# Optimization experiments

Measured on AMD Instinct MI355X. Metric: run time of the kernel, lower is better.

The kernel has to match this reference:

```python
import jax, jax.numpy as jnp
import numpy as np

B, S, HID = 1, 1024, 4096
NH, NKV, HD = 32, 8, 128
GROUPS = NH // NKV
THETA = 10000.0
SPAR = 0.5          # sparse_aggression (layer_idx > 0)
MIN_IDX = 4         # min_sparse_index: always-kept sink tokens
NEG = jnp.float32(-1e30)


def setup_inputs() -> dict:
    key = jax.random.key(0)
    k0, k1, k2, k3, k4 = jax.random.split(key, 5)
    sc = 0.02
    return {
        "hidden_states": jax.random.normal(k0, (B, S, HID), jnp.float32),
        "position_ids": jnp.arange(S, dtype=jnp.int32)[None, :],
        "Wq": jax.random.normal(k1, (NH * HD, HID), jnp.float32) * sc,
        "Wk": jax.random.normal(k2, (NKV * HD, HID), jnp.float32) * sc,
        "Wv": jax.random.normal(k3, (NKV * HD, HID), jnp.float32) * sc,
        "Wo": jax.random.normal(k4, (HID, NH * HD), jnp.float32) * sc,
    }


def _rotate_half(x):
    h = x.shape[-1] // 2
    return jnp.concatenate([-x[..., h:], x[..., :h]], axis=-1)


def _rope_cos_sin(position_ids):
    inv_freq = 1.0 / (THETA ** (jnp.arange(0, HD, 2, dtype=jnp.float32) / HD))
    freqs = position_ids.astype(jnp.float32)[..., None] * inv_freq  # [B,S,HD/2]
    emb = jnp.concatenate([freqs, freqs], axis=-1)                  # [B,S,HD]
    return jnp.cos(emb)[:, None], jnp.sin(emb)[:, None]             # [B,1,S,HD]


def reference(hidden_states, position_ids, Wq, Wk, Wv, Wo):
    b, s, _ = hidden_states.shape
    # QKV projections (nn.Linear: x @ W.T)
    q = (hidden_states @ Wq.T).reshape(b, s, NH, HD).transpose(0, 2, 1, 3)
    k = (hidden_states @ Wk.T).reshape(b, s, NKV, HD).transpose(0, 2, 1, 3)
    v = (hidden_states @ Wv.T).reshape(b, s, NKV, HD).transpose(0, 2, 1, 3)
    # RoPE
    cos, sin = _rope_cos_sin(position_ids)
    q = q * cos + _rotate_half(q) * sin
    k = k * cos + _rotate_half(k) * sin
    # repeat_kv (GQA expansion)
    k = jnp.repeat(k, GROUPS, axis=1)
    v = jnp.repeat(v, GROUPS, axis=1)
    # causal additive mask [1,1,S,S]
    causal = jnp.where(jnp.triu(jnp.ones((s, s), bool), 1), NEG, jnp.float32(0))[None, None]
    scale = 1.0 / np.sqrt(HD)
    scores = jnp.einsum('bhqd,bhkd->bhqk', q, k) * scale
    # oracle importance: softmax of (softmaxed) masked attention (no_grad in original)
    oracle = jax.nn.softmax((scores + causal).astype(jnp.float32), axis=-1)
    importance = jax.nn.softmax(oracle, axis=-1)
    importance = jax.lax.stop_gradient(importance)
    # descending sort -> rank of each key for each query
    sorted_idx = jnp.argsort(-importance, axis=-1)          # [B,H,S,S]
    ranks = jnp.argsort(sorted_idx, axis=-1)                # inverse perm
    # per-query token budget: keep ceil-ish top-k proportional to row length
    k_per_row = jnp.maximum((SPAR * (jnp.arange(s) + 1)).astype(jnp.int32), 1)
    key_idx = jnp.arange(s)
    kept = (ranks < k_per_row[None, None, :, None]) | (key_idx[None, None, None, :] < MIN_IDX)
    sparse_mask = jnp.where(kept, jnp.float32(0), NEG)
    # sparse attention
    attn = scores + sparse_mask + causal
    probs = jax.nn.softmax(attn.astype(jnp.float32), axis=-1).astype(v.dtype)
    out = jnp.einsum('bhqk,bhkd->bhqd', probs, v)           # [B,H,S,HD]
    out = out.transpose(0, 2, 1, 3).reshape(b, s, NH * HD)
    return out @ Wo.T
```

## Files before the change

kernel.cpp:

```cpp
#include <hip/hip_runtime.h>
#include <hip/hip_bf16.h>

#define S_LEN 1024
#define HID   4096
#define NH    32
#define NKV   8
#define HD    128
#define MIN_IDX 4
#define AO_COLS 4096
#define HEAD_STRIDE 131072

typedef __attribute__((ext_vector_type(8))) short short8;
typedef __attribute__((ext_vector_type(4))) float f32x4;

__device__ __forceinline__ unsigned short f2bf(float f) {
  union { float f; unsigned u; } v; v.f = f;
  unsigned r = v.u + 0x7FFFu + ((v.u >> 16) & 1u);
  return (unsigned short)(r >> 16);
}
__device__ __forceinline__ float bf2f(unsigned short h) {
  union { unsigned u; float f; } v; v.u = ((unsigned)h) << 16;
  return v.f;
}
__device__ __forceinline__ unsigned pk2(float a, float b) {
  union { __hip_bfloat162 h; unsigned u; } c;
  c.h = __float22bfloat162_rn(make_float2(a, b));
  return c.u;
}
__device__ __forceinline__ short8 pack8(float4 a, float4 b) {
  union { short8 s; unsigned u[4]; } r;
  r.u[0] = pk2(a.x, a.y); r.u[1] = pk2(a.z, a.w);
  r.u[2] = pk2(b.x, b.y); r.u[3] = pk2(b.z, b.w);
  return r.s;
}
__device__ __forceinline__ unsigned ordf(float f) {
  union { float f; int i; } v; v.f = f;
  return (unsigned)(v.i ^ ((v.i >> 31) | 0x80000000));
}
__device__ __forceinline__ float iordf(unsigned u) {
  union { int i; float f; } v;
  v.i = (u & 0x80000000u) ? (int)(u ^ 0x80000000u) : (int)~u;
  return v.f;
}
__device__ __forceinline__ float wave_sum_f(float v) {
  #pragma unroll
  for (int m = 32; m >= 1; m >>= 1) v += __shfl_xor(v, m);
  return v;
}
__device__ __forceinline__ unsigned wave_max_u(unsigned v) {
  #pragma unroll
  for (int m = 32; m >= 1; m >>= 1) { unsigned o = __shfl_xor(v, m); v = o > v ? o : v; }
  return v;
}
__device__ __forceinline__ void wave_lds_fence() {
  __builtin_amdgcn_s_waitcnt(0xC07F);
  __builtin_amdgcn_wave_barrier();
}
__device__ __forceinline__ void gload_lds16(const unsigned short* g, unsigned short* l) {
  auto gp = (const __attribute__((address_space(1))) unsigned*)g;
  auto lp = (__attribute__((address_space(3))) unsigned*)(unsigned)(unsigned long long)l;
  __builtin_amdgcn_global_load_lds(gp, lp, 16, 0, 0);
}

__global__ __launch_bounds__(256) void cvt_k(
    const float* __restrict__ src, unsigned short* __restrict__ dst)
{
  const size_t i = ((size_t)blockIdx.x * 256 + threadIdx.x) * 8;
  float4 a = *(const float4*)(src + i);
  float4 b = *(const float4*)(src + i + 4);
  *(short8*)(dst + i) = pack8(a, b);
}

__global__ __launch_bounds__(256) void gemm_qkv_k(
    const unsigned short* __restrict__ Xb, const unsigned short* __restrict__ Wb,
    unsigned short* __restrict__ Qraw, unsigned short* __restrict__ Kraw,
    unsigned short* __restrict__ Vt)
{
  __shared__ unsigned short As[128 * 32];
  __shared__ unsigned short Bs[128 * 32];
  const int nt = blockIdx.x;
  const int n0 = nt * 128;
  const int m0 = blockIdx.y * 128;
  const int t = threadIdx.x, w = t >> 6, lane = t & 63;
  const int wm = w >> 1, wn = w & 1;
  const int mcol = lane & 15, quad = lane >> 4;
  const int lrow = lane >> 2, lcol = (lane & 3) * 8;

  const unsigned short* Ag = Xb + (size_t)m0 * HID;
  const unsigned short* Bg = Wb + (size_t)n0 * HID;

  f32x4 acc[4][4];
  #pragma unroll
  for (int i = 0; i < 4; i++)
    #pragma unroll
    for (int j = 0; j < 4; j++) acc[i][j] = (f32x4){0.f, 0.f, 0.f, 0.f};

  for (int k0 = 0; k0 < HID; k0 += 32) {
    #pragma unroll
    for (int c2 = 0; c2 < 2; c2++) {
      const int c = w * 2 + c2;
      gload_lds16(Ag + (size_t)(c*16 + lrow) * HID + k0 + lcol, &As[c * 512]);
      gload_lds16(Bg + (size_t)(c*16 + lrow) * HID + k0 + lcol, &Bs[c * 512]);
    }
    __syncthreads();
    short8 af[4], bf[4];
    #pragma unroll
    for (int i = 0; i < 4; i++) af[i] = *(const short8*)&As[(wm*64 + i*16 + mcol)*32 + quad*8];
    #pragma unroll
    for (int j = 0; j < 4; j++) bf[j] = *(const short8*)&Bs[(wn*64 + j*16 + mcol)*32 + quad*8];
    #pragma unroll
    for (int i = 0; i < 4; i++)
      #pragma unroll
      for (int j = 0; j < 4; j++)
        acc[i][j] = __builtin_amdgcn_mfma_f32_16x16x32_bf16(af[i], bf[j], acc[i][j], 0, 0, 0);
    __syncthreads();
  }

  if (nt < 40) {
    unsigned short* dst = (nt < 32) ? (Qraw + (size_t)nt * HEAD_STRIDE)
                                    : (Kraw + (size_t)(nt - 32) * HEAD_STRIDE);
    #pragma unroll
    for (int i = 0; i < 4; i++) {
      const int rb = m0 + wm*64 + i*16 + quad*4;
      #pragma unroll
      for (int j = 0; j < 4; j++) {
        const int d = wn*64 + j*16 + mcol;
        #pragma unroll
        for (int r = 0; r < 4; r++)
          dst[(size_t)(rb + r) * HD + d] = f2bf(acc[i][j][r]);
      }
    }
  } else {
    unsigned short* dst = Vt + (size_t)(nt - 40) * HEAD_STRIDE;
    #pragma unroll
    for (int i = 0; i < 4; i++) {
      const int rb = m0 + wm*64 + i*16 + quad*4;
      #pragma unroll
      for (int j = 0; j < 4; j++) {
        const int d = wn*64 + j*16 + mcol;
        ushort4 v4;
        v4.x = f2bf(acc[i][j][0]); v4.y = f2bf(acc[i][j][1]);
        v4.z = f2bf(acc[i][j][2]); v4.w = f2bf(acc[i][j][3]);
        *(ushort4*)(dst + (size_t)d * S_LEN + rb) = v4;
      }
    }
  }
}

__global__ __launch_bounds__(256) void rope_qk_k(
    const int* __restrict__ pos_ids,
    unsigned short* __restrict__ Qraw, unsigned short* __restrict__ Kraw)
{
  const int w = threadIdx.x >> 6, lane = threadIdx.x & 63;
  const int gw = blockIdx.x * 4 + w;
  const int hidx = gw >> 10;
  const int s = gw & 1023;
  const float pos = (float)pos_ids[s];
  const float invf = powf(10000.0f, -(float)lane * (1.0f / 64.0f));
  float sn, cs;
  sincosf(pos * invf, &sn, &cs);
  unsigned short* base = (hidx < NH)
      ? (Qraw + (size_t)hidx * HEAD_STRIDE + (size_t)s * HD)
      : (Kraw + (size_t)(hidx - NH) * HEAD_STRIDE + (size_t)s * HD);
  const float x0 = bf2f(base[lane]), x1 = bf2f(base[lane + 64]);
  base[lane]      = f2bf(x0 * cs - x1 * sn);
  base[lane + 64] = f2bf(x1 * cs + x0 * sn);
}

#define PSTR 1040
template<int KT>
__device__ __forceinline__ void attn_body(
    const unsigned short* __restrict__ Qb, const unsigned short* __restrict__ Kh,
    const unsigned short* __restrict__ Vh, unsigned short* __restrict__ AO,
    unsigned short (*Pl)[PSTR], unsigned (*hist)[256], float* rowinv,
    int q0, int h, int w, int lane, int mcol, int quad)
{
  constexpr int NC = 2 * KT;
  const float scale = 0.08838834764831845f;
  float (*scb)[16][130] = (float (*)[16][130])&Pl[0][0];

  short8 aq[4];
  {
    const unsigned short* qrow = Qb + ((size_t)h * S_LEN + q0 + mcol) * HD + quad * 8;
    #pragma unroll
    for (int kk = 0; kk < 4; kk++) aq[kk] = *(const short8*)(qrow + kk * 32);
  }

  unsigned su[4][NC];

  #pragma unroll
  for (int kt = 0; kt < KT; kt++) {
    short8 bfr[2][4];
    #pragma unroll
    for (int g2 = 0; g2 < 2; g2++) {
      const int key = kt * 128 + (w * 2 + g2) * 16 + mcol;
      const unsigned short* krow = Kh + (size_t)key * HD + quad * 8;
      #pragma unroll
      for (int kk = 0; kk < 4; kk++) bfr[g2][kk] = *(const short8*)(krow + kk * 32);
    }
    f32x4 d4[2];
    d4[0] = (f32x4){0.f,0.f,0.f,0.f}; d4[1] = (f32x4){0.f,0.f,0.f,0.f};
    #pragma unroll
    for (int g2 = 0; g2 < 2; g2++)
      #pragma unroll
      for (int kk = 0; kk < 4; kk++)
        d4[g2] = __builtin_amdgcn_mfma_f32_16x16x32_bf16(aq[kk], bfr[g2][kk], d4[g2], 0, 0, 0);
    #pragma unroll
    for (int g2 = 0; g2 < 2; g2++) {
      const int colc = (w * 2 + g2) * 16 + mcol;
      #pragma unroll
      for (int r = 0; r < 4; r++) scb[kt & 1][quad*4 + r][colc] = d4[g2][r] * scale;
    }
    __syncthreads();
    #pragma unroll
    for (int i = 0; i < 4; i++)
      #pragma unroll
      for (int sub = 0; sub < 2; sub++)
        su[i][kt*2 + sub] = ordf(scb[kt & 1][w*4 + i][sub*64 + lane]);
  }
  __syncthreads();

  const unsigned long long lmlt = (1ull << lane) - 1ull;
  int Lr[4], krem[4], tot[4];
  unsigned prefix[4];
  #pragma unroll
  for (int i = 0; i < 4; i++) {
    Lr[i] = q0 + w*4 + i + 1;
    int ks = Lr[i] >> 1; if (ks < 1) ks = 1;
    krem[i] = ks; tot[i] = Lr[i]; prefix[i] = 0u;
  }

  unsigned msk = 0u;
  #pragma unroll
  for (int pass = 0; pass < 2; pass++) {
    const int shift = 24 - pass * 8;
    #pragma unroll
    for (int p = 0; p < 2; p++) {
      { uint4 z = {0u, 0u, 0u, 0u}; *(uint4*)&hist[w][lane * 4] = z; }
      wave_lds_fence();
      #pragma unroll
      for (int c = 0; c < NC; c++) {
        const int j = c * 64 + lane;
        #pragma unroll
        for (int rr = 0; rr < 2; rr++) {
          const int i = p * 2 + rr;
          if (j < Lr[i] && (su[i][c] & msk) == prefix[i])
            atomicAdd(&hist[w][(su[i][c] >> shift) & 255], 1u << (16 * rr));
        }
      }
      wave_lds_fence();
      const uint4 cv = *(const uint4*)&hist[w][252 - lane * 4];
      unsigned c4[4] = { cv.w, cv.z, cv.y, cv.x };
      const unsigned lsum = c4[0] + c4[1] + c4[2] + c4[3];
      unsigned x = lsum;
      #pragma unroll
      for (int d2 = 1; d2 < 64; d2 <<= 1) { unsigned y = __shfl_up(x, d2); if (lane >= d2) x += y; }
      const unsigned runp = x - lsum;
      #pragma unroll
      for (int rr = 0; rr < 2; rr++) {
        const int i = p * 2 + rr;
        const int sh16 = 16 * rr;
        int run = (int)((runp >> sh16) & 0xFFFFu);
        int fbin = -1, fbefore = 0, fcnt = 0;
        #pragma unroll
        for (int j2 = 0; j2 < 4; j2++) {
          const int cnum = (int)((c4[j2] >> sh16) & 0xFFFFu);
          if (fbin < 0 && run < krem[i] && run + cnum >= krem[i]) {
            fbin = 255 - lane*4 - j2; fbefore = run; fcnt = cnum;
          }
          run += cnum;
        }
        const unsigned long long bal = __ballot(fbin >= 0);
        int bin = 0, before = 0, cnt = krem[i];
        if (bal != 0ull) {
          const int srcl = __ffsll((unsigned long long)bal) - 1;
          bin = __shfl(fbin, srcl);
          before = __shfl(fbefore, srcl);
          cnt = __shfl(fcnt, srcl);
          if (bin < 0) bin = 0;
        }
        krem[i] -= before; if (krem[i] < 1) krem[i] = 1;
        tot[i] = cnt;
        prefix[i] |= ((unsigned)bin) << shift;
      }
    }
    msk |= 0xFFu << (24 - pass * 8);
  }

  #pragma unroll
  for (int i = 0; i < 4; i++) {
    const int r = w * 4 + i;
    const int L = Lr[i];
    unsigned btau = prefix[i];
    unsigned bmsk = 0xFFFF0000u;
    int kr = krem[i];
    int tt = tot[i];
    #pragma unroll 1
    for (int b = 15; b >= 0; --b) {
      if (tt <= kr) break;
      const unsigned bit = 1u << b;
      const unsigned am = bmsk | bit;
      const unsigned test = btau | bit;
      int cnt = 0;
      #pragma unroll
      for (int c = 0; c < NC; c++) {
        const int j = c * 64 + lane;
        cnt += (int)__popcll(__ballot(j < L && (su[i][c] & am) == test));
      }
      if (cnt >= kr) { btau = test; tt = cnt; }
      else           { kr -= cnt; tt -= cnt; }
      bmsk = am;
    }

    unsigned um = 0;
    #pragma unroll
    for (int c = 0; c < NC; c++) {
      const int j = c * 64 + lane;
      if (j < L && su[i][c] > um) um = su[i][c];
    }
    const float mx = iordf(wave_max_u(um));

    float ssum = 0.f;
    int tiebase = 0;
    #pragma unroll
    for (int c = 0; c < NC; c++) {
      const int j = c * 64 + lane;
      const unsigned u = su[i][c];
      const unsigned umv = u & bmsk;
      const bool eq = (j < L) && (umv == btau);
      const unsigned long long bal = __ballot(eq);
      const int trank = tiebase + (int)__popcll(bal & lmlt);
      tiebase += (int)__popcll(bal);
      const bool kept = (j < L) &&
          ((umv > btau) || (eq && trank < kr) || (j < MIN_IDX));
      const float e = kept ? __expf(iordf(u) - mx) : 0.f;
      Pl[r][c*64 + lane] = f2bf(e);
      ssum += e;
    }
    ssum = wave_sum_f(ssum);
    if (lane == 0) rowinv[r] = 1.f / fmaxf(ssum, 1e-30f);
  }
  __syncthreads();

  f32x4 opv[2];
  opv[0] = (f32x4){0.f,0.f,0.f,0.f}; opv[1] = (f32x4){0.f,0.f,0.f,0.f};
  #pragma unroll
  for (int kt = 0; kt < KT; kt++) {
    #pragma unroll
    for (int kb = 0; kb < 4; kb++) {
      short8 af = *(const short8*)&Pl[mcol][kt*128 + kb*32 + quad*8];
      #pragma unroll
      for (int n2 = 0; n2 < 2; n2++) {
        const int d = (w*2 + n2) * 16 + mcol;
        short8 bfr = *(const short8*)(Vh + (size_t)d * S_LEN + kt*128 + kb*32 + quad*8);
        opv[n2] = __builtin_amdgcn_mfma_f32_16x16x32_bf16(af, bfr, opv[n2], 0, 0, 0);
      }
    }
  }
  #pragma unroll
  for (int n2 = 0; n2 < 2; n2++) {
    const int col = h * HD + (w*2 + n2) * 16 + mcol;
    #pragma unroll
    for (int r2 = 0; r2 < 4; r2++) {
      const int row = q0 + quad*4 + r2;
      AO[(size_t)row * AO_COLS + col] = f2bf(opv[n2][r2] * rowinv[quad*4 + r2]);
    }
  }
}

__global__ __launch_bounds__(256, 4) void attn_k(
    const unsigned short* __restrict__ Qb, const unsigned short* __restrict__ Kb,
    const unsigned short* __restrict__ Vt, unsigned short* __restrict__ AO)
{
  __shared__ unsigned short Pl[16][PSTR];
  __shared__ unsigned hist[4][256];
  __shared__ float rowinv[16];
  const int rb = (int)gridDim.x - 1 - (int)blockIdx.x;
  const int h = blockIdx.y;
  const int kvh = h >> 2;
  const int q0 = rb * 16;
  const int kt_max = (rb >> 3) + 1;
  const int t = threadIdx.x, w = t >> 6, lane = t & 63;
  const int mcol = lane & 15, quad = lane >> 4;
  const unsigned short* Kh = Kb + (size_t)kvh * HEAD_STRIDE;
  const unsigned short* Vh = Vt + (size_t)kvh * HEAD_STRIDE;

  switch (kt_max) {
    case 1: attn_body<1>(Qb, Kh, Vh, AO, Pl, hist, rowinv, q0, h, w, lane, mcol, quad); break;
    case 2: attn_body<2>(Qb, Kh, Vh, AO, Pl, hist, rowinv, q0, h, w, lane, mcol, quad); break;
    case 3: attn_body<3>(Qb, Kh, Vh, AO, Pl, hist, rowinv, q0, h, w, lane, mcol, quad); break;
    case 4: attn_body<4>(Qb, Kh, Vh, AO, Pl, hist, rowinv, q0, h, w, lane, mcol, quad); break;
    case 5: attn_body<5>(Qb, Kh, Vh, AO, Pl, hist, rowinv, q0, h, w, lane, mcol, quad); break;
    case 6: attn_body<6>(Qb, Kh, Vh, AO, Pl, hist, rowinv, q0, h, w, lane, mcol, quad); break;
    case 7: attn_body<7>(Qb, Kh, Vh, AO, Pl, hist, rowinv, q0, h, w, lane, mcol, quad); break;
    default: attn_body<8>(Qb, Kh, Vh, AO, Pl, hist, rowinv, q0, h, w, lane, mcol, quad); break;
  }
}

__global__ __launch_bounds__(256) void gemm_out_k(
    const unsigned short* __restrict__ A, const unsigned short* __restrict__ Wob,
    float* __restrict__ Out)
{
  __shared__ unsigned short As[128 * 32];
  __shared__ unsigned short Bs[128 * 32];
  const int n0 = blockIdx.x * 128;
  const int m0 = blockIdx.y * 128;
  const int t = threadIdx.x, w = t >> 6, lane = t & 63;
  const int wm = w >> 1, wn = w & 1;
  const int mcol = lane & 15, quad = lane >> 4;
  const int lrow = lane >> 2, lcol = (lane & 3) * 8;

  const unsigned short* Ag = A   + (size_t)m0 * AO_COLS;
  const unsigned short* Bg = Wob + (size_t)n0 * AO_COLS;

  f32x4 acc[4][4];
  #pragma unroll
  for (int i = 0; i < 4; i++)
    #pragma unroll
    for (int j = 0; j < 4; j++) acc[i][j] = (f32x4){0.f, 0.f, 0.f, 0.f};

  for (int k0 = 0; k0 < AO_COLS; k0 += 32) {
    #pragma unroll
    for (int c2 = 0; c2 < 2; c2++) {
      const int c = w * 2 + c2;
      gload_lds16(Ag + (size_t)(c*16 + lrow) * AO_COLS + k0 + lcol, &As[c * 512]);
      gload_lds16(Bg + (size_t)(c*16 + lrow) * AO_COLS + k0 + lcol, &Bs[c * 512]);
    }
    __syncthreads();
    short8 af[4], bf[4];
    #pragma unroll
    for (int i = 0; i < 4; i++) af[i] = *(const short8*)&As[(wm*64 + i*16 + mcol)*32 + quad*8];
    #pragma unroll
    for (int j = 0; j < 4; j++) bf[j] = *(const short8*)&Bs[(wn*64 + j*16 + mcol)*32 + quad*8];
    #pragma unroll
    for (int i = 0; i < 4; i++)
      #pragma unroll
      for (int j = 0; j < 4; j++)
        acc[i][j] = __builtin_amdgcn_mfma_f32_16x16x32_bf16(af[i], bf[j], acc[i][j], 0, 0, 0);
    __syncthreads();
  }
  #pragma unroll
  for (int i = 0; i < 4; i++) {
    const int rb = m0 + wm*64 + i*16 + quad*4;
    #pragma unroll
    for (int j = 0; j < 4; j++) {
      const int col = n0 + wn*64 + j*16 + mcol;
      #pragma unroll
      for (int r = 0; r < 4; r++)
        Out[(size_t)(rb + r) * HID + col] = acc[i][j][r];
    }
  }
}

extern "C" void kernel_launch(void* const* d_in, const int* in_sizes, int n_in,
                              void* d_out, int out_size, void* d_ws, size_t ws_size,
                              hipStream_t stream) {
  (void)in_sizes; (void)n_in; (void)out_size; (void)ws_size;
  const float* X   = (const float*)d_in[0];
  const int*   pos = (const int*)d_in[1];
  const float* Wq  = (const float*)d_in[2];
  const float* Wk  = (const float*)d_in[3];
  const float* Wv  = (const float*)d_in[4];
  const float* Wo  = (const float*)d_in[5];
  float* out = (float*)d_out;

  char* ws = (char*)d_ws;
  unsigned short* Qraw  = (unsigned short*)ws;
  unsigned short* Kraw  = (unsigned short*)(ws + 8388608);
  unsigned short* Vt    = (unsigned short*)(ws + 10485760);
  unsigned short* AO    = (unsigned short*)(ws + 12582912);
  unsigned short* Xb    = (unsigned short*)(ws + 20971520);
  unsigned short* Wqkvb = (unsigned short*)(ws + 29360128);
  unsigned short* Wob   = Wqkvb;

  cvt_k<<<dim3(2048), dim3(256), 0, stream>>>(X,  Xb);
  cvt_k<<<dim3(8192), dim3(256), 0, stream>>>(Wq, Wqkvb);
  cvt_k<<<dim3(2048), dim3(256), 0, stream>>>(Wk, Wqkvb + 16777216);
  cvt_k<<<dim3(2048), dim3(256), 0, stream>>>(Wv, Wqkvb + 20971520);

  gemm_qkv_k<<<dim3(48, 8),  dim3(256), 0, stream>>>(Xb, Wqkvb, Qraw, Kraw, Vt);
  rope_qk_k <<<dim3(10240),  dim3(256), 0, stream>>>(pos, Qraw, Kraw);

  cvt_k<<<dim3(8192), dim3(256), 0, stream>>>(Wo, Wob);

  attn_k    <<<dim3(64, 32), dim3(256), 0, stream>>>(Qraw, Kraw, Vt, AO);
  gemm_out_k<<<dim3(32, 8),  dim3(256), 0, stream>>>(AO, Wob, out);
}
```

Before: 537.2 us.

## Triple-buffer GEMM loads, fuse input conversions, and tighten radix top-k select

Both GEMM kernels move to a three-stage LDS ring with async global-to-LDS loads issued two tiles ahead. This replaces the two syncthreads per k-step with one vmcnt wait and one barrier, so memory latency overlaps with MFMA work. The four fp32-to-bf16 conversion launches become one kernel that picks its source by block index, saving launch overhead. The top-k radix select in attention now uses three 6-bit passes with a lane-replicated histogram to cut atomic contention, and skips rows whose threshold is already resolved. The cost is more LDS per GEMM block, which may lower occupancy, plus more complex select logic.

New measurement: 456.4 us. 15.0% less time.

```diff
diff --git a/kernel.cpp b/kernel.cpp
--- a/kernel.cpp
+++ b/kernel.cpp
@@ -71,13 +71,30 @@
   *(short8*)(dst + i) = pack8(a, b);
 }
 
+__global__ __launch_bounds__(256) void cvt4_k(
+    const float* __restrict__ s0, const float* __restrict__ s1,
+    const float* __restrict__ s2, const float* __restrict__ s3,
+    unsigned short* __restrict__ d0, unsigned short* __restrict__ d1)
+{
+  const int b = blockIdx.x;
+  const float* src; unsigned short* dst; int rb;
+  if (b < 2048)       { src = s0; dst = d0;            rb = b; }
+  else if (b < 10240) { src = s1; dst = d1;            rb = b - 2048; }
+  else if (b < 12288) { src = s2; dst = d1 + 16777216; rb = b - 10240; }
+  else                { src = s3; dst = d1 + 20971520; rb = b - 12288; }
+  const size_t i = ((size_t)rb * 256 + threadIdx.x) * 8;
+  float4 a = *(const float4*)(src + i);
+  float4 c = *(const float4*)(src + i + 4);
+  *(short8*)(dst + i) = pack8(a, c);
+}
+
 __global__ __launch_bounds__(256) void gemm_qkv_k(
     const unsigned short* __restrict__ Xb, const unsigned short* __restrict__ Wb,
     unsigned short* __restrict__ Qraw, unsigned short* __restrict__ Kraw,
     unsigned short* __restrict__ Vt)
 {
-  __shared__ unsigned short As[128 * 32];
-  __shared__ unsigned short Bs[128 * 32];
+  __shared__ unsigned short As[3][128 * 32];
+  __shared__ unsigned short Bs[3][128 * 32];
   const int nt = blockIdx.x;
   const int n0 = nt * 128;
   const int m0 = blockIdx.y * 128;
@@ -95,25 +112,39 @@
     #pragma unroll
     for (int j = 0; j < 4; j++) acc[i][j] = (f32x4){0.f, 0.f, 0.f, 0.f};
 
-  for (int k0 = 0; k0 < HID; k0 += 32) {
-    #pragma unroll
-    for (int c2 = 0; c2 < 2; c2++) {
-      const int c = w * 2 + c2;
-      gload_lds16(Ag + (size_t)(c*16 + lrow) * HID + k0 + lcol, &As[c * 512]);
-      gload_lds16(Bg + (size_t)(c*16 + lrow) * HID + k0 + lcol, &Bs[c * 512]);
-    }
-    __syncthreads();
+  constexpr int NT = HID / 32;
+  #define STAGE_QKV(buf, k0)                                                  \
+    { const int c0 = w * 2, c1 = w * 2 + 1;                                   \
+      gload_lds16(Ag + (size_t)(c0*16 + lrow) * HID + (k0) + lcol, &As[buf][c0 * 512]); \
+      gload_lds16(Bg + (size_t)(c0*16 + lrow) * HID + (k0) + lcol, &Bs[buf][c0 * 512]); \
+      gload_lds16(Ag + (size_t)(c1*16 + lrow) * HID + (k0) + lcol, &As[buf][c1 * 512]); \
+      gload_lds16(Bg + (size_t)(c1*16 + lrow) * HID + (k0) + lcol, &Bs[buf][c1 * 512]); }
+
+  STAGE_QKV(0, 0)
+  STAGE_QKV(1, 32)
+  asm volatile("s_waitcnt vmcnt(4)" ::: "memory");
+  __builtin_amdgcn_s_barrier();
+  __builtin_amdgcn_sched_barrier(0);
+
+  int cur = 0, stg = 2;
+  for (int kt = 0; kt < NT; ++kt) {
+    if (kt + 2 < NT) STAGE_QKV(stg, (kt + 2) * 32)
     short8 af[4], bf[4];
     #pragma unroll
-    for (int i = 0; i < 4; i++) af[i] = *(const short8*)&As[(wm*64 + i*16 + mcol)*32 + quad*8];
-    #pragma unroll
-    for (int j = 0; j < 4; j++) bf[j] = *(const short8*)&Bs[(wn*64 + j*16 + mcol)*32 + quad*8];
+    for (int i = 0; i < 4; i++) af[i] = *(const short8*)&As[cur][(wm*64 + i*16 + mcol)*32 + quad*8];
+    #pragma unroll
+    for (int j = 0; j < 4; j++) bf[j] = *(const short8*)&Bs[cur][(wn*64 + j*16 + mcol)*32 + quad*8];
     #pragma unroll
     for (int i = 0; i < 4; i++)
       #pragma unroll
       for (int j = 0; j < 4; j++)
         acc[i][j] = __builtin_amdgcn_mfma_f32_16x16x32_bf16(af[i], bf[j], acc[i][j], 0, 0, 0);
-    __syncthreads();
+    if (kt + 2 < NT) { asm volatile("s_waitcnt vmcnt(4)" ::: "memory"); }
+    else             { asm volatile("s_waitcnt vmcnt(0)" ::: "memory"); }
+    __builtin_amdgcn_s_barrier();
+    __builtin_amdgcn_sched_barrier(0);
+    cur = (cur == 2) ? 0 : cur + 1;
+    stg = (stg == 2) ? 0 : stg + 1;
   }
 
   if (nt < 40) {
@@ -221,21 +252,23 @@
   __syncthreads();
 
   const unsigned long long lmlt = (1ull << lane) - 1ull;
+  const int rep = lane & 3;
   int Lr[4], krem[4], tot[4];
-  unsigned prefix[4];
+  unsigned prefix[4], pmsk[4];
   #pragma unroll
   for (int i = 0; i < 4; i++) {
     Lr[i] = q0 + w*4 + i + 1;
     int ks = Lr[i] >> 1; if (ks < 1) ks = 1;
-    krem[i] = ks; tot[i] = Lr[i]; prefix[i] = 0u;
-  }
-
-  unsigned msk = 0u;
-  #pragma unroll
-  for (int pass = 0; pass < 2; pass++) {
-    const int shift = 24 - pass * 8;
+    krem[i] = ks; tot[i] = Lr[i]; prefix[i] = 0u; pmsk[i] = 0u;
+  }
+
+  #pragma unroll
+  for (int pass = 0; pass < 3; pass++) {
+    const int shift = 26 - pass * 6;
     #pragma unroll
     for (int p = 0; p < 2; p++) {
+      const int i0 = p*2, i1 = p*2 + 1;
+      if (tot[i0] <= krem[i0] && tot[i1] <= krem[i1]) continue;
       { uint4 z = {0u, 0u, 0u, 0u}; *(uint4*)&hist[w][lane * 4] = z; }
       wave_lds_fence();
       #pragma unroll
@@ -244,47 +277,39 @@
         #pragma unroll
         for (int rr = 0; rr < 2; rr++) {
           const int i = p * 2 + rr;
-          if (j < Lr[i] && (su[i][c] & msk) == prefix[i])
-            atomicAdd(&hist[w][(su[i][c] >> shift) & 255], 1u << (16 * rr));
+          if (tot[i] > krem[i] && j < Lr[i] && (su[i][c] & pmsk[i]) == prefix[i])
+            atomicAdd(&hist[w][((su[i][c] >> shift) & 63) * 4 + rep], 1u << (16 * rr));
         }
       }
       wave_lds_fence();
-      const uint4 cv = *(const uint4*)&hist[w][252 - lane * 4];
-      unsigned c4[4] = { cv.w, cv.z, cv.y, cv.x };
-      const unsigned lsum = c4[0] + c4[1] + c4[2] + c4[3];
-      unsigned x = lsum;
+      const uint4 cv = *(const uint4*)&hist[w][(63 - lane) * 4];
+      const unsigned cnt2 = cv.x + cv.y + cv.z + cv.w;
+      unsigned x = cnt2;
       #pragma unroll
       for (int d2 = 1; d2 < 64; d2 <<= 1) { unsigned y = __shfl_up(x, d2); if (lane >= d2) x += y; }
-      const unsigned runp = x - lsum;
+      const unsigned runp = x - cnt2;
       #pragma unroll
       for (int rr = 0; rr < 2; rr++) {
         const int i = p * 2 + rr;
+        if (tot[i] <= krem[i]) continue;
         const int sh16 = 16 * rr;
-        int run = (int)((runp >> sh16) & 0xFFFFu);
-        int fbin = -1, fbefore = 0, fcnt = 0;
-        #pragma unroll
-        for (int j2 = 0; j2 < 4; j2++) {
-          const int cnum = (int)((c4[j2] >> sh16) & 0xFFFFu);
-          if (fbin < 0 && run < krem[i] && run + cnum >= krem[i]) {
-            fbin = 255 - lane*4 - j2; fbefore = run; fcnt = cnum;
-          }
-          run += cnum;
-        }
-        const unsigned long long bal = __ballot(fbin >= 0);
-        int bin = 0, before = 0, cnt = krem[i];
-        if (bal != 0ull) {
-          const int srcl = __ffsll((unsigned long long)bal) - 1;
-          bin = __shfl(fbin, srcl);
-          before = __shfl(fbefore, srcl);
-          cnt = __shfl(fcnt, srcl);
-          if (bin < 0) bin = 0;
-        }
-        krem[i] -= before; if (krem[i] < 1) krem[i] = 1;
-        tot[i] = cnt;
+        const int run = (int)((runp >> sh16) & 0xFFFFu);
+        const int cn  = (int)((cnt2 >> sh16) & 0xFFFFu);
+        const bool hit = (run < krem[i]) && (run + cn >= krem[i]);
+        unsigned packv = hit ? (((unsigned)(63 - lane) << 22) |
+                                ((unsigned)run << 11) | (unsigned)cn) : 0u;
+        const unsigned long long bal = __ballot(hit);
+        const int srcl = __ffsll(bal) - 1;
+        const unsigned res = __shfl(packv, srcl);
+        const int bin = res >> 22;
+        const int before = (res >> 11) & 0x7FF;
+        const int cn2 = res & 0x7FF;
+        krem[i] -= before;
+        tot[i] = cn2;
         prefix[i] |= ((unsigned)bin) << shift;
+        pmsk[i] |= 63u << shift;
       }
     }
-    msk |= 0xFFu << (24 - pass * 8);
   }
 
   #pragma unroll
@@ -292,11 +317,12 @@
     const int r = w * 4 + i;
     const int L = Lr[i];
     unsigned btau = prefix[i];
-    unsigned bmsk = 0xFFFF0000u;
+    unsigned bmsk = pmsk[i];
     int kr = krem[i];
     int tt = tot[i];
+    const int bs = (bmsk == 0u) ? 31 : (__builtin_ctz(bmsk) - 1);
     #pragma unroll 1
-    for (int b = 15; b >= 0; --b) {
+    for (int b = bs; b >= 0; --b) {
       if (tt <= kr) break;
       const unsigned bit = 1u << b;
       const unsigned am = bmsk | bit;
@@ -401,8 +427,8 @@
     const unsigned short* __restrict__ A, const unsigned short* __restrict__ Wob,
     float* __restrict__ Out)
 {
-  __shared__ unsigned short As[128 * 32];
-  __shared__ unsigned short Bs[128 * 32];
+  __shared__ unsigned short As[3][128 * 32];
+  __shared__ unsigned short Bs[3][128 * 32];
   const int n0 = blockIdx.x * 128;
   const int m0 = blockIdx.y * 128;
   const int t = threadIdx.x, w = t >> 6, lane = t & 63;
@@ -419,26 +445,41 @@
     #pragma unroll
     for (int j = 0; j < 4; j++) acc[i][j] = (f32x4){0.f, 0.f, 0.f, 0.f};
 
-  for (int k0 = 0; k0 < AO_COLS; k0 += 32) {
-    #pragma unroll
-    for (int c2 = 0; c2 < 2; c2++) {
-      const int c = w * 2 + c2;
-      gload_lds16(Ag + (size_t)(c*16 + lrow) * AO_COLS + k0 + lcol, &As[c * 512]);
-      gload_lds16(Bg + (size_t)(c*16 + lrow) * AO_COLS + k0 + lcol, &Bs[c * 512]);
-    }
-    __syncthreads();
+  constexpr int NT = AO_COLS / 32;
+  #define STAGE_OUT(buf, k0)                                                  \
+    { const int c0 = w * 2, c1 = w * 2 + 1;                                   \
+      gload_lds16(Ag + (size_t)(c0*16 + lrow) * AO_COLS + (k0) + lcol, &As[buf][c0 * 512]); \
+      gload_lds16(Bg + (size_t)(c0*16 + lrow) * AO_COLS + (k0) + lcol, &Bs[buf][c0 * 512]); \
+      gload_lds16(Ag + (size_t)(c1*16 + lrow) * AO_COLS + (k0) + lcol, &As[buf][c1 * 512]); \
+      gload_lds16(Bg + (size_t)(c1*16 + lrow) * AO_COLS + (k0) + lcol, &Bs[buf][c1 * 512]); }
+
+  STAGE_OUT(0, 0)
+  STAGE_OUT(1, 32)
+  asm volatile("s_waitcnt vmcnt(4)" ::: "memory");
+  __builtin_amdgcn_s_barrier();
+  __builtin_amdgcn_sched_barrier(0);
+
+  int cur = 0, stg = 2;
+  for (int kt = 0; kt < NT; ++kt) {
+    if (kt + 2 < NT) STAGE_OUT(stg, (kt + 2) * 32)
     short8 af[4], bf[4];
     #pragma unroll
-    for (int i = 0; i < 4; i++) af[i] = *(const short8*)&As[(wm*64 + i*16 + mcol)*32 + quad*8];
-    #pragma unroll
-    for (int j = 0; j < 4; j++) bf[j] = *(const short8*)&Bs[(wn*64 + j*16 + mcol)*32 + quad*8];
+    for (int i = 0; i < 4; i++) af[i] = *(const short8*)&As[cur][(wm*64 + i*16 + mcol)*32 + quad*8];
+    #pragma unroll
+    for (int j = 0; j < 4; j++) bf[j] = *(const short8*)&Bs[cur][(wn*64 + j*16 + mcol)*32 + quad*8];
     #pragma unroll
     for (int i = 0; i < 4; i++)
       #pragma unroll
       for (int j = 0; j < 4; j++)
         acc[i][j] = __builtin_amdgcn_mfma_f32_16x16x32_bf16(af[i], bf[j], acc[i][j], 0, 0, 0);
-    __syncthreads();
-  }
+    if (kt + 2 < NT) { asm volatile("s_waitcnt vmcnt(4)" ::: "memory"); }
+    else             { asm volatile("s_waitcnt vmcnt(0)" ::: "memory"); }
+    __builtin_amdgcn_s_barrier();
+    __builtin_amdgcn_sched_barrier(0);
+    cur = (cur == 2) ? 0 : cur + 1;
+    stg = (stg == 2) ? 0 : stg + 1;
+  }
+
   #pragma unroll
   for (int i = 0; i < 4; i++) {
     const int rb = m0 + wm*64 + i*16 + quad*4;
@@ -473,10 +514,7 @@
   unsigned short* Wqkvb = (unsigned short*)(ws + 29360128);
   unsigned short* Wob   = Wqkvb;
 
-  cvt_k<<<dim3(2048), dim3(256), 0, stream>>>(X,  Xb);
-  cvt_k<<<dim3(8192), dim3(256), 0, stream>>>(Wq, Wqkvb);
-  cvt_k<<<dim3(2048), dim3(256), 0, stream>>>(Wk, Wqkvb + 16777216);
-  cvt_k<<<dim3(2048), dim3(256), 0, stream>>>(Wv, Wqkvb + 20971520);
+  cvt4_k<<<dim3(14336), dim3(256), 0, stream>>>(X, Wq, Wk, Wv, Xb, Wqkvb);
 
   gemm_qkv_k<<<dim3(48, 8),  dim3(256), 0, stream>>>(Xb, Wqkvb, Qraw, Kraw, Vt);
   rope_qk_k <<<dim3(10240),  dim3(256), 0, stream>>>(pos, Qraw, Kraw);
```
